# Optimization experiments

Measured on AMD Instinct MI355X. Metric: run time of the kernel, lower is better.

The kernel has to match this reference:

```python
import jax, jax.numpy as jnp
import numpy as np

N_LAYERS = 3
HIDDEN = 128
N_NODES = 50000
N_EDGES = 800000
NEG_SLOPE = 0.2  # PyG GATConv default negative_slope
EPS = 1e-16      # PyG softmax denominator eps


def setup_inputs() -> dict:
    key = jax.random.key(0)
    ks = jax.random.split(key, 6)
    z = jax.random.normal(ks[0], (N_NODES, HIDDEN), dtype=jnp.float32)
    edge_index = jax.random.randint(ks[1], (2, N_EDGES), 0, N_NODES, dtype=jnp.int32)
    scale = 1.0 / np.sqrt(HIDDEN)
    Ws = jax.random.normal(ks[2], (N_LAYERS, HIDDEN, HIDDEN), dtype=jnp.float32) * scale
    a_src = jax.random.normal(ks[3], (N_LAYERS, HIDDEN), dtype=jnp.float32) * scale
    a_dst = jax.random.normal(ks[4], (N_LAYERS, HIDDEN), dtype=jnp.float32) * scale
    bias = jnp.zeros((N_LAYERS, HIDDEN), dtype=jnp.float32)
    return {"z": z, "edge_index": edge_index, "Ws": Ws, "a_src": a_src,
            "a_dst": a_dst, "bias": bias}


def _gat_conv(h, W, a_s, a_d, b, src, dst):
    # Linear transform: [N, D]
    x = h @ W
    # Per-node attention logits, gathered per edge
    alpha_s = x @ a_s  # [N]
    alpha_d = x @ a_d  # [N]
    e = jax.nn.leaky_relu(alpha_s[src] + alpha_d[dst], NEG_SLOPE)  # [E]
    # Segment softmax over incoming edges of each destination node
    e_max = jax.ops.segment_max(e, dst, num_segments=N_NODES)
    ex = jnp.exp(e - e_max[dst])
    denom = jax.ops.segment_sum(ex, dst, num_segments=N_NODES)
    alpha = ex / (denom[dst] + EPS)  # [E]
    # Weighted scatter-aggregation of source features
    out = jax.ops.segment_sum(x[src] * alpha[:, None], dst, num_segments=N_NODES)
    return out + b


def reference(z, edge_index, Ws, a_src, a_dst, bias):
    # add_self_loops=True (PyG GATConv default)
    loop = jnp.arange(N_NODES, dtype=edge_index.dtype)
    src = jnp.concatenate([edge_index[0], loop])
    dst = jnp.concatenate([edge_index[1], loop])
    h = z
    for l in range(N_LAYERS):
        h = _gat_conv(h, Ws[l], a_src[l], a_dst[l], bias[l], src, dst)
        if l < N_LAYERS - 1:
            h = jax.nn.relu(h)
    return h
```

## Files before the change

kernel.cpp:

```cpp
#include <hip/hip_runtime.h>

#define NN 50000
#define HID 128
#define HH (HID * HID)
#define NE 800000
#define ET (NE + NN)
#define NEG_SLOPE 0.2f
#define CAP 64
#define WTOT (3 * HID * HID)
#define VTOT (3 * 3 * HID)
#define SCHUNK 1024
#define SCAT_VB (((ET + SCHUNK - 1) / SCHUNK) * 8)
#define GEMM_VB ((NN + 63) / 64)
#define WL3 (3 * HH)

typedef __attribute__((ext_vector_type(8))) short short8v;
typedef __attribute__((ext_vector_type(4))) float f32x4;

__device__ inline float b2f(unsigned short u) {
    union { unsigned int i; float f; } x; x.i = ((unsigned int)u) << 16; return x.f;
}
__device__ inline float f_lo(unsigned int u) {
    union { unsigned int i; float f; } x; x.i = u << 16; return x.f;
}
__device__ inline float f_hi(unsigned int u) {
    union { unsigned int i; float f; } x; x.i = u & 0xFFFF0000u; return x.f;
}
__device__ inline unsigned short f2b(float f) {
    unsigned int x; __builtin_memcpy(&x, &f, 4);
    unsigned int lsb = (x >> 16) & 1u;
    x += 0x7fffu + lsb;
    return (unsigned short)(x >> 16);
}
__device__ inline void splitbf(float v, unsigned short& hi, unsigned short& lo) {
    hi = f2b(v);
    lo = f2b(v - b2f(hi));
}
__device__ inline float readlane_f(float v, int l) {
    union { float f; int i; } x; x.f = v;
    x.i = __builtin_amdgcn_readlane(x.i, l);
    return x.f;
}
__device__ __forceinline__ int probe_hf_dev(const unsigned short* z, int t, int* sflag) {
    if (t < 64) {
        unsigned short a = z[t * 4];
        unsigned short b = z[t * 4 + 2];
        int ea = (a >> 7) & 0xFF, eb = (b >> 7) & 0xFF;
        int w1 = (ea >= 0x9A || (ea <= 0x30 && a != 0)) ? 1 : 0;
        int w2 = (eb >= 0x9A || (eb <= 0x30 && b != 0)) ? 1 : 0;
        int wild = __popcll(__ballot(w1)) + __popcll(__ballot(w2));
        if (t == 0) *sflag = (wild < 8) ? 1 : 0;
    }
    __syncthreads();
    return *sflag;
}

__global__ __launch_bounds__(256) void prep(
        const unsigned short* __restrict__ z, const void* __restrict__ Ws,
        const void* __restrict__ as_, const void* __restrict__ ad_,
        const void* __restrict__ b_, unsigned short* __restrict__ Wb,
        float* __restrict__ asf, float* __restrict__ adf, float* __restrict__ bff,
        int* __restrict__ pos) {
    __shared__ int sflag;
    const int t = threadIdx.x;
    const int f = probe_hf_dev(z, t, &sflag);
    const int gtid = blockIdx.x * 256 + t;
    if (gtid < NN) pos[gtid] = 0;
    if (gtid < WTOT) {
        int L = gtid >> 14, k = (gtid >> 7) & 127, n = gtid & 127;
        float v = f ? b2f(((const unsigned short*)Ws)[gtid]) : ((const float*)Ws)[gtid];
        unsigned short hi, lo;
        splitbf(v, hi, lo);
        unsigned short* hbase = Wb + (size_t)L * WL3;
        int bo = (n * 256 + k * 2) ^ ((n & 7) << 4);
        *(unsigned short*)((char*)hbase + bo) = hi;
        hbase[HH + n * HID + k]     = lo;
        hbase[2 * HH + n * HID + k] = hi;
    } else {
        int i = gtid - WTOT;
        if (i < VTOT) {
            int which = i / (3 * HID), j = i - which * (3 * HID);
            const void* in = which == 0 ? as_ : which == 1 ? ad_ : b_;
            float* o = which == 0 ? asf : which == 1 ? adf : bff;
            o[j] = f ? b2f(((const unsigned short*)in)[j]) : ((const float*)in)[j];
        }
    }
}

__global__ __launch_bounds__(256) void scat_gemm0(
        const unsigned short* __restrict__ z, const int* __restrict__ ei,
        const unsigned short* __restrict__ Wb, const float* __restrict__ a_s,
        const float* __restrict__ a_d, int* __restrict__ pos, int* __restrict__ csr,
        unsigned short* __restrict__ x, float* __restrict__ als, float* __restrict__ ald) {
    __shared__ unsigned short Wh[HH];
    __shared__ int sflag;
    const int t = threadIdx.x;
    const int hf = probe_hf_dev(z, t, &sflag);

    if (blockIdx.x < SCAT_VB) {
        const int rng  = blockIdx.x & 7;
        const int base = (blockIdx.x >> 3) * SCHUNK;
#pragma unroll
        for (int k = 0; k < SCHUNK / 256; ++k) {
            int e = base + k * 256 + t;
            if (e >= ET) continue;
            int d = (e < NE) ? ei[NE + e] : (e - NE);
            if ((d * 8) / NN != rng) continue;
            int s = (e < NE) ? ei[e] : d;
            int slot = atomicAdd(&pos[d], 1);
            if (slot < CAP) csr[(d << 6) + slot] = s;
        }
        return;
    }

    const int base = (blockIdx.x - SCAT_VB) * 64;
    const unsigned short* Wlo = Wb + HH;
#pragma unroll
    for (int i = 0; i < 8; ++i) {
        int c = i * 256 + t;
        ((short8v*)Wh)[c] = ((const short8v*)Wb)[c];
    }
    __syncthreads();

    const int w  = t >> 6;
    const int l  = t & 63;
    const int lr = l & 15;
    const int lk = l >> 4;
    const int arow = base + w * 16 + lr;
    const bool rowok = (arow < NN);

    const short8v zv = (short8v){0, 0, 0, 0, 0, 0, 0, 0};
    short8v ahi[4], alo[4];
    if (hf) {
        const unsigned short* hp = z + (size_t)arow * HID + lk * 8;
#pragma unroll
        for (int ks = 0; ks < 4; ++ks) {
            ahi[ks] = rowok ? *(const short8v*)(hp + ks * 32) : zv;
            alo[ks] = zv;
        }
    } else {
        const float* hp = (const float*)z + (size_t)arow * HID + lk * 8;
#pragma unroll
        for (int ks = 0; ks < 4; ++ks) {
            float4 v0 = make_float4(0.f, 0.f, 0.f, 0.f), v1 = v0;
            if (rowok) {
                v0 = *(const float4*)(hp + ks * 32);
                v1 = *(const float4*)(hp + ks * 32 + 4);
            }
            ushort4 h0, l0, h1, l1;
            splitbf(v0.x, h0.x, l0.x); splitbf(v0.y, h0.y, l0.y);
            splitbf(v0.z, h0.z, l0.z); splitbf(v0.w, h0.w, l0.w);
            splitbf(v1.x, h1.x, l1.x); splitbf(v1.y, h1.y, l1.y);
            splitbf(v1.z, h1.z, l1.z); splitbf(v1.w, h1.w, l1.w);
            ahi[ks] = (short8v){(short)h0.x, (short)h0.y, (short)h0.z, (short)h0.w,
                                (short)h1.x, (short)h1.y, (short)h1.z, (short)h1.w};
            alo[ks] = (short8v){(short)l0.x, (short)l0.y, (short)l0.z, (short)l0.w,
                                (short)l1.x, (short)l1.y, (short)l1.z, (short)l1.w};
        }
    }

    f32x4 acc[8];
#pragma unroll
    for (int nt = 0; nt < 8; ++nt) acc[nt] = (f32x4){0.f, 0.f, 0.f, 0.f};

#pragma unroll
    for (int ks = 0; ks < 4; ++ks) {
#pragma unroll
        for (int nt = 0; nt < 8; ++nt) {
            int row = nt * 16 + lr;
            int bo = (row * 256 + ks * 64 + lk * 16) ^ ((lr & 7) << 4);
            short8v bhi = *(const short8v*)((const char*)Wh + bo);
            short8v blo = *(const short8v*)(Wlo + row * HID + ks * 32 + lk * 8);
            acc[nt] = __builtin_amdgcn_mfma_f32_16x16x32_bf16(ahi[ks], bhi, acc[nt], 0, 0, 0);
            if (!hf) acc[nt] = __builtin_amdgcn_mfma_f32_16x16x32_bf16(alo[ks], bhi, acc[nt], 0, 0, 0);
            acc[nt] = __builtin_amdgcn_mfma_f32_16x16x32_bf16(ahi[ks], blo, acc[nt], 0, 0, 0);
        }
    }

    float ps[4] = {0.f, 0.f, 0.f, 0.f};
    float pd[4] = {0.f, 0.f, 0.f, 0.f};
#pragma unroll
    for (int nt = 0; nt < 8; ++nt) {
        float asv = a_s[nt * 16 + lr];
        float adv = a_d[nt * 16 + lr];
#pragma unroll
        for (int r = 0; r < 4; ++r) {
            ps[r] = fmaf(acc[nt][r], asv, ps[r]);
            pd[r] = fmaf(acc[nt][r], adv, pd[r]);
        }
    }
#pragma unroll
    for (int m = 8; m >= 1; m >>= 1) {
#pragma unroll
        for (int r = 0; r < 4; ++r) {
            ps[r] += __shfl_xor(ps[r], m, 16);
            pd[r] += __shfl_xor(pd[r], m, 16);
        }
    }
#pragma unroll
    for (int r = 0; r < 4; ++r) {
        int grow = base + w * 16 + lk * 4 + r;
        if (grow < NN) {
#pragma unroll
            for (int nt = 0; nt < 8; ++nt)
                x[(size_t)grow * HID + nt * 16 + lr] = f2b(acc[nt][r]);
            if (lr == 0) { als[grow] = ps[r]; ald[grow] = pd[r]; }
        }
    }
}

__global__ __launch_bounds__(256, 4) void agg_gemm(
        const unsigned short* __restrict__ xin, const int* __restrict__ deg_,
        const int* __restrict__ csr, const float* __restrict__ als_in,
        const float* __restrict__ ald_in, const float* __restrict__ bias,
        const unsigned short* __restrict__ Whip, const unsigned short* __restrict__ Wlop,
        const float* __restrict__ a_s, const float* __restrict__ a_d,
        unsigned short* __restrict__ xout, float* __restrict__ als_out,
        float* __restrict__ ald_out) {
    __shared__ unsigned short Ah[64 * HID];
    __shared__ unsigned short Al[64 * HID];
    const int t = threadIdx.x;
    const int base = blockIdx.x * 64;
    const int w = t >> 6;
    const int lane = t & 63;
    const unsigned int* x2 = (const unsigned int*)xin;
    const float2 bv = ((const float2*)bias)[lane];

    for (int i = 0; i < 16; ++i) {
        const int node = base + w * 16 + i;
        const int deg = (node < NN) ? min(deg_[node], CAP) : 0;
        int   sidx = 0;
        float p    = 0.f;
        if (lane < deg) {
            sidx = csr[(node << 6) + lane];
            float e = als_in[sidx] + ald_in[node];
            e = fmaxf(e, NEG_SLOPE * e);
            e = fminf(e, 60.f);
            p = __expf(e);
        }
        float den = p;
#pragma unroll
        for (int m = 1; m < 64; m <<= 1) den += __shfl_xor(den, m);
        p *= 1.f / (den + 1e-16f);

        float ax = 0.f, ay = 0.f;
#pragma unroll
        for (int j0 = 0; j0 < CAP; j0 += 16) {
            if (j0 >= deg) break;
            unsigned int u[16]; float pj[16];
#pragma unroll
            for (int k = 0; k < 16; ++k) {
                const int j = j0 + k;
                int ijs = __builtin_amdgcn_readlane(sidx, j);
                pj[k] = readlane_f(p, j);
                const unsigned int* rowp = x2 + (((size_t)(unsigned)ijs) << 6);
                u[k] = rowp[lane];
            }
#pragma unroll
            for (int k = 0; k < 16; ++k) {
                ax = fmaf(pj[k], f_lo(u[k]), ax);
                ay = fmaf(pj[k], f_hi(u[k]), ay);
            }
        }
        float ox = fmaxf(ax + bv.x, 0.f);
        float oy = fmaxf(ay + bv.y, 0.f);
        unsigned short hx, lx, hy, ly;
        splitbf(ox, hx, lx); splitbf(oy, hy, ly);
        const int r = w * 16 + i;
        const int bo = (r * 256 + lane * 4) ^ ((r & 7) << 4);
        ushort2 ph; ph.x = hx; ph.y = hy;
        ushort2 pl; pl.x = lx; pl.y = ly;
        *(ushort2*)((char*)Ah + bo) = ph;
        *(ushort2*)((char*)Al + bo) = pl;
    }
    __syncthreads();

    const int lr = lane & 15;
    const int lk = lane >> 4;
    const int ar = w * 16 + lr;
    short8v ahi[4], alo[4];
#pragma unroll
    for (int ks = 0; ks < 4; ++ks) {
        int ab = (ar * 256 + ks * 64 + lk * 16) ^ ((ar & 7) << 4);
        ahi[ks] = *(const short8v*)((const char*)Ah + ab);
        alo[ks] = *(const short8v*)((const char*)Al + ab);
    }

    f32x4 acc[8];
#pragma unroll
    for (int nt = 0; nt < 8; ++nt) acc[nt] = (f32x4){0.f, 0.f, 0.f, 0.f};

#pragma unroll
    for (int ks = 0; ks < 4; ++ks) {
#pragma unroll
        for (int nt = 0; nt < 8; ++nt) {
            int row = nt * 16 + lr;
            short8v bhi = *(const short8v*)(Whip + row * HID + ks * 32 + lk * 8);
            short8v blo = *(const short8v*)(Wlop + row * HID + ks * 32 + lk * 8);
            acc[nt] = __builtin_amdgcn_mfma_f32_16x16x32_bf16(ahi[ks], bhi, acc[nt], 0, 0, 0);
            acc[nt] = __builtin_amdgcn_mfma_f32_16x16x32_bf16(alo[ks], bhi, acc[nt], 0, 0, 0);
            acc[nt] = __builtin_amdgcn_mfma_f32_16x16x32_bf16(ahi[ks], blo, acc[nt], 0, 0, 0);
        }
    }

    float ps[4] = {0.f, 0.f, 0.f, 0.f};
    float pd[4] = {0.f, 0.f, 0.f, 0.f};
#pragma unroll
    for (int nt = 0; nt < 8; ++nt) {
        float asv = a_s[nt * 16 + lr];
        float adv = a_d[nt * 16 + lr];
#pragma unroll
        for (int r = 0; r < 4; ++r) {
            ps[r] = fmaf(acc[nt][r], asv, ps[r]);
            pd[r] = fmaf(acc[nt][r], adv, pd[r]);
        }
    }
#pragma unroll
    for (int m = 8; m >= 1; m >>= 1) {
#pragma unroll
        for (int r = 0; r < 4; ++r) {
            ps[r] += __shfl_xor(ps[r], m, 16);
            pd[r] += __shfl_xor(pd[r], m, 16);
        }
    }
#pragma unroll
    for (int r = 0; r < 4; ++r) {
        int grow = base + w * 16 + lk * 4 + r;
        if (grow < NN) {
#pragma unroll
            for (int nt = 0; nt < 8; ++nt)
                xout[(size_t)grow * HID + nt * 16 + lr] = f2b(acc[nt][r]);
            if (lr == 0) { als_out[grow] = ps[r]; ald_out[grow] = pd[r]; }
        }
    }
}

__global__ __launch_bounds__(256) void agg_fin(
        const unsigned short* __restrict__ z, const unsigned short* __restrict__ x,
        const int* __restrict__ deg_, const int* __restrict__ csr,
        const float* __restrict__ als, const float* __restrict__ ald,
        const float* __restrict__ bias, void* __restrict__ out) {
    __shared__ int sflag;
    const int t = threadIdx.x;
    const int hf = probe_hf_dev(z, t, &sflag);
    const int node = (blockIdx.x * 256 + t) >> 6;
    const int lane = t & 63;
    if (node >= NN) return;
    const int deg = min(deg_[node], CAP);

    int   sidx = 0;
    float p    = 0.f;
    if (lane < deg) {
        sidx = csr[(node << 6) + lane];
        float e = als[sidx] + ald[node];
        e = fmaxf(e, NEG_SLOPE * e);
        e = fminf(e, 60.f);
        p = __expf(e);
    }
    float den = p;
#pragma unroll
    for (int m = 1; m < 64; m <<= 1) den += __shfl_xor(den, m);
    p *= 1.f / (den + 1e-16f);

    const unsigned int* x2 = (const unsigned int*)x;
    float ax = 0.f, ay = 0.f;
#pragma unroll
    for (int j0 = 0; j0 < CAP; j0 += 16) {
        if (j0 >= deg) break;
        unsigned int u[16]; float pj[16];
#pragma unroll
        for (int k = 0; k < 16; ++k) {
            const int j = j0 + k;
            int ijs = __builtin_amdgcn_readlane(sidx, j);
            pj[k] = readlane_f(p, j);
            const unsigned int* rowp = x2 + (((size_t)(unsigned)ijs) << 6);
            u[k] = rowp[lane];
        }
#pragma unroll
        for (int k = 0; k < 16; ++k) {
            ax = fmaf(pj[k], f_lo(u[k]), ax);
            ay = fmaf(pj[k], f_hi(u[k]), ay);
        }
    }

    float2 bv = ((const float2*)bias)[lane];
    float ox = ax + bv.x;
    float oy = ay + bv.y;
    if (hf) {
        ushort2 pk; pk.x = f2b(ox); pk.y = f2b(oy);
        *(ushort2*)((unsigned short*)out + (size_t)node * HID + lane * 2) = pk;
    } else {
        ((float2*)out)[(size_t)node * 64 + lane] = make_float2(ox, oy);
    }
}

extern "C" void kernel_launch(void* const* d_in, const int* in_sizes, int n_in,
                              void* d_out, int out_size, void* d_ws, size_t ws_size,
                              hipStream_t stream) {
    const unsigned short* z  = (const unsigned short*)d_in[0];
    const int*            ei = (const int*)d_in[1];
    const void*           Ws = d_in[2];
    const void*           as = d_in[3];
    const void*           ad = d_in[4];
    const void*           bb = d_in[5];

    char* wsp = (char*)d_ws;
    auto alloc = [&](size_t bytes) -> char* {
        char* p = wsp; wsp += (bytes + 255) & ~(size_t)255; return p;
    };
    int*            pos  = (int*)alloc(NN * 4);
    int*            csrp = (int*)alloc((size_t)NN * CAP * 4);
    float*          alsA = (float*)alloc(NN * 4);
    float*          aldA = (float*)alloc(NN * 4);
    float*          alsB = (float*)alloc(NN * 4);
    float*          aldB = (float*)alloc(NN * 4);
    unsigned short* Wb   = (unsigned short*)alloc((size_t)3 * WL3 * 2);
    float*          asf  = (float*)alloc(3 * HID * 4);
    float*          adf  = (float*)alloc(3 * HID * 4);
    float*          bff  = (float*)alloc(3 * HID * 4);
    unsigned short* xb0  = (unsigned short*)alloc((size_t)NN * HID * 2);
    unsigned short* xb1  = (unsigned short*)alloc((size_t)NN * HID * 2);

    prep<<<197, 256, 0, stream>>>(z, Ws, as, ad, bb, Wb, asf, adf, bff, pos);

    scat_gemm0<<<SCAT_VB + GEMM_VB, 256, 0, stream>>>(z, ei, Wb, asf, adf,
                                                      pos, csrp, xb0, alsA, aldA);

    agg_gemm<<<GEMM_VB, 256, 0, stream>>>(xb0, pos, csrp, alsA, aldA, bff,
                                          Wb + WL3 + 2 * HH, Wb + WL3 + HH,
                                          asf + HID, adf + HID, xb1, alsB, aldB);

    agg_gemm<<<GEMM_VB, 256, 0, stream>>>(xb1, pos, csrp, alsB, aldB, bff + HID,
                                          Wb + 2 * WL3 + 2 * HH, Wb + 2 * WL3 + HH,
                                          asf + 2 * HID, adf + 2 * HID, xb0, alsA, aldA);

    agg_fin<<<(NN + 3) / 4, 256, 0, stream>>>(z, xb0, pos, csrp, alsA, aldA,
                                              bff + 2 * HID, d_out);
}
```

Before: 314.3 us.

## Retile fused aggregate-GEMM to 32-node blocks with 8 waves splitting output columns

Each agg_gemm block now covers 32 nodes with 512 threads (8 waves) instead of 64 nodes with 256 threads. Each wave aggregates 4 nodes rather than 16. In the GEMM phase the waves form a 2x4 grid, so each wave computes a 16-row by 32-column tile rather than 16x128. The attention-logit partial sums from the four column-waves are combined through shared memory behind an extra barrier. The aim is more parallelism and less serial gather work per wave, fewer accumulator registers, and half the LDS per block. The cost is an extra sync and more blocks, each of which re-reads the weight slices.

```diff
diff --git a/kernel.cpp b/kernel.cpp
--- a/kernel.cpp
+++ b/kernel.cpp
@@ -12,6 +12,7 @@
 #define SCHUNK 1024
 #define SCAT_VB (((ET + SCHUNK - 1) / SCHUNK) * 8)
 #define GEMM_VB ((NN + 63) / 64)
+#define AG_VB ((NN + 31) / 32)
 #define WL3 (3 * HH)
 
 typedef __attribute__((ext_vector_type(8))) short short8v;
@@ -209,7 +210,7 @@
     }
 }
 
-__global__ __launch_bounds__(256, 4) void agg_gemm(
+__global__ __launch_bounds__(512) void agg_gemm(
         const unsigned short* __restrict__ xin, const int* __restrict__ deg_,
         const int* __restrict__ csr, const float* __restrict__ als_in,
         const float* __restrict__ ald_in, const float* __restrict__ bias,
@@ -217,17 +218,19 @@
         const float* __restrict__ a_s, const float* __restrict__ a_d,
         unsigned short* __restrict__ xout, float* __restrict__ als_out,
         float* __restrict__ ald_out) {
-    __shared__ unsigned short Ah[64 * HID];
-    __shared__ unsigned short Al[64 * HID];
+    __shared__ unsigned short Ah[32 * HID];
+    __shared__ unsigned short Al[32 * HID];
+    __shared__ float aps[32][4], apd[32][4];
     const int t = threadIdx.x;
-    const int base = blockIdx.x * 64;
+    const int base = blockIdx.x * 32;
     const int w = t >> 6;
     const int lane = t & 63;
     const unsigned int* x2 = (const unsigned int*)xin;
     const float2 bv = ((const float2*)bias)[lane];
 
-    for (int i = 0; i < 16; ++i) {
-        const int node = base + w * 16 + i;
+    for (int i = 0; i < 4; ++i) {
+        const int r = w * 4 + i;
+        const int node = base + r;
         const int deg = (node < NN) ? min(deg_[node], CAP) : 0;
         int   sidx = 0;
         float p    = 0.f;
@@ -266,7 +269,6 @@
         float oy = fmaxf(ay + bv.y, 0.f);
         unsigned short hx, lx, hy, ly;
         splitbf(ox, hx, lx); splitbf(oy, hy, ly);
-        const int r = w * 16 + i;
         const int bo = (r * 256 + lane * 4) ^ ((r & 7) << 4);
         ushort2 ph; ph.x = hx; ph.y = hy;
         ushort2 pl; pl.x = lx; pl.y = ly;
@@ -275,9 +277,11 @@
     }
     __syncthreads();
 
+    const int wr = w & 1;
+    const int wc = w >> 1;
     const int lr = lane & 15;
     const int lk = lane >> 4;
-    const int ar = w * 16 + lr;
+    const int ar = wr * 16 + lr;
     short8v ahi[4], alo[4];
 #pragma unroll
     for (int ks = 0; ks < 4; ++ks) {
@@ -286,15 +290,15 @@
         alo[ks] = *(const short8v*)((const char*)Al + ab);
     }
 
-    f32x4 acc[8];
-#pragma unroll
-    for (int nt = 0; nt < 8; ++nt) acc[nt] = (f32x4){0.f, 0.f, 0.f, 0.f};
+    f32x4 acc[2];
+#pragma unroll
+    for (int nt = 0; nt < 2; ++nt) acc[nt] = (f32x4){0.f, 0.f, 0.f, 0.f};
 
 #pragma unroll
     for (int ks = 0; ks < 4; ++ks) {
 #pragma unroll
-        for (int nt = 0; nt < 8; ++nt) {
-            int row = nt * 16 + lr;
+        for (int nt = 0; nt < 2; ++nt) {
+            int row = wc * 32 + nt * 16 + lr;
             short8v bhi = *(const short8v*)(Whip + row * HID + ks * 32 + lk * 8);
             short8v blo = *(const short8v*)(Wlop + row * HID + ks * 32 + lk * 8);
             acc[nt] = __builtin_amdgcn_mfma_f32_16x16x32_bf16(ahi[ks], bhi, acc[nt], 0, 0, 0);
@@ -306,9 +310,9 @@
     float ps[4] = {0.f, 0.f, 0.f, 0.f};
     float pd[4] = {0.f, 0.f, 0.f, 0.f};
 #pragma unroll
-    for (int nt = 0; nt < 8; ++nt) {
-        float asv = a_s[nt * 16 + lr];
-        float adv = a_d[nt * 16 + lr];
+    for (int nt = 0; nt < 2; ++nt) {
+        float asv = a_s[wc * 32 + nt * 16 + lr];
+        float adv = a_d[wc * 32 + nt * 16 + lr];
 #pragma unroll
         for (int r = 0; r < 4; ++r) {
             ps[r] = fmaf(acc[nt][r], asv, ps[r]);
@@ -323,14 +327,28 @@
             pd[r] += __shfl_xor(pd[r], m, 16);
         }
     }
+    if (lr == 0) {
+#pragma unroll
+        for (int r = 0; r < 4; ++r) {
+            int rib = wr * 16 + lk * 4 + r;
+            aps[rib][wc] = ps[r];
+            apd[rib][wc] = pd[r];
+        }
+    }
+    __syncthreads();
+
 #pragma unroll
     for (int r = 0; r < 4; ++r) {
-        int grow = base + w * 16 + lk * 4 + r;
+        int rib = wr * 16 + lk * 4 + r;
+        int grow = base + rib;
         if (grow < NN) {
 #pragma unroll
-            for (int nt = 0; nt < 8; ++nt)
-                xout[(size_t)grow * HID + nt * 16 + lr] = f2b(acc[nt][r]);
-            if (lr == 0) { als_out[grow] = ps[r]; ald_out[grow] = pd[r]; }
+            for (int nt = 0; nt < 2; ++nt)
+                xout[(size_t)grow * HID + wc * 32 + nt * 16 + lr] = f2b(acc[nt][r]);
+            if (wc == 0 && lr == 0) {
+                als_out[grow] = (aps[rib][0] + aps[rib][1]) + (aps[rib][2] + aps[rib][3]);
+                ald_out[grow] = (apd[rib][0] + apd[rib][1]) + (apd[rib][2] + apd[rib][3]);
+            }
         }
     }
 }
@@ -426,13 +444,13 @@
     scat_gemm0<<<SCAT_VB + GEMM_VB, 256, 0, stream>>>(z, ei, Wb, asf, adf,
                                                       pos, csrp, xb0, alsA, aldA);
 
-    agg_gemm<<<GEMM_VB, 256, 0, stream>>>(xb0, pos, csrp, alsA, aldA, bff,
-                                          Wb + WL3 + 2 * HH, Wb + WL3 + HH,
-                                          asf + HID, adf + HID, xb1, alsB, aldB);
-
-    agg_gemm<<<GEMM_VB, 256, 0, stream>>>(xb1, pos, csrp, alsB, aldB, bff + HID,
-                                          Wb + 2 * WL3 + 2 * HH, Wb + 2 * WL3 + HH,
-                                          asf + 2 * HID, adf + 2 * HID, xb0, alsA, aldA);
+    agg_gemm<<<AG_VB, 512, 0, stream>>>(xb0, pos, csrp, alsA, aldA, bff,
+                                        Wb + WL3 + 2 * HH, Wb + WL3 + HH,
+                                        asf + HID, adf + HID, xb1, alsB, aldB);
+
+    agg_gemm<<<AG_VB, 512, 0, stream>>>(xb1, pos, csrp, alsB, aldB, bff + HID,
+                                        Wb + 2 * WL3 + 2 * HH, Wb + 2 * WL3 + HH,
+                                        asf + 2 * HID, adf + 2 * HID, xb0, alsA, aldA);
 
     agg_fin<<<(NN + 3) / 4, 256, 0, stream>>>(z, xb0, pos, csrp, alsA, aldA,
                                               bff + 2 * HID, d_out);
```

Result: faster. 289.0 us (-8.1%).
